# Optimization experiments

Measured on AMD Instinct MI355X. Metric: run time of the kernel, lower is better.

Reference implementation:

```python
import jax, jax.numpy as jnp
import numpy as np

WIN = (8, 8)
HEADS = 6
DIM = 192
N_TOK = WIN[0] * WIN[1]


def _cpb_coords_table():
    # (2*Wh-1, 2*Ww-1, 2) log-spaced continuous relative coords, flattened to (T, 2)
    h = np.arange(-(WIN[0] - 1), WIN[0], dtype=np.float32)
    w = np.arange(-(WIN[1] - 1), WIN[1], dtype=np.float32)
    t = np.stack(np.meshgrid(h, w, indexing='ij'), axis=-1)
    t[..., 0] /= WIN[0] - 1
    t[..., 1] /= WIN[1] - 1
    t *= 8.0
    t = np.sign(t) * np.log2(np.abs(t) + 1.0) / np.log2(8.0)
    return jnp.asarray(t.reshape(-1, 2))


def _rel_pos_index():
    ch, cw = np.meshgrid(np.arange(WIN[0]), np.arange(WIN[1]), indexing='ij')
    cf = np.stack([ch.ravel(), cw.ravel()])  # (2, N)
    rc = (cf[:, :, None] - cf[:, None, :]).transpose(1, 2, 0)  # (N, N, 2)
    rc[..., 0] += WIN[0] - 1
    rc[..., 1] += WIN[1] - 1
    rc[..., 0] *= 2 * WIN[1] - 1
    return jnp.asarray(rc.sum(-1).ravel())  # (N*N,)


_COORDS = _cpb_coords_table()
_RPI = _rel_pos_index()


def setup_inputs() -> dict:
    key = jax.random.key(0)
    ks = jax.random.split(key, 8)
    B_ = 4096
    x = jax.random.normal(ks[0], (B_, N_TOK, DIM), dtype=jnp.float32)
    mask = jnp.zeros((64, N_TOK, N_TOK), dtype=jnp.float32)
    qkv_w = jax.random.normal(ks[1], (3 * DIM, DIM), dtype=jnp.float32) * 0.02
    q_bias = jnp.zeros((DIM,), dtype=jnp.float32)
    v_bias = jnp.zeros((DIM,), dtype=jnp.float32)
    logit_scale = jnp.log(10.0) * jnp.ones((HEADS, 1, 1), dtype=jnp.float32)
    cpb_w1 = jax.random.normal(ks[2], (512, 2), dtype=jnp.float32) * 0.02
    cpb_b1 = jnp.zeros((512,), dtype=jnp.float32)
    cpb_w2 = jax.random.normal(ks[3], (HEADS, 512), dtype=jnp.float32) * 0.02
    proj_w = jax.random.normal(ks[4], (DIM, DIM), dtype=jnp.float32) * 0.02
    proj_b = jnp.zeros((DIM,), dtype=jnp.float32)
    return {"x": x, "mask": mask, "qkv_w": qkv_w, "q_bias": q_bias, "v_bias": v_bias,
            "logit_scale": logit_scale, "cpb_w1": cpb_w1, "cpb_b1": cpb_b1,
            "cpb_w2": cpb_w2, "proj_w": proj_w, "proj_b": proj_b}


def reference(x, mask, qkv_w, q_bias, v_bias, logit_scale, cpb_w1, cpb_b1, cpb_w2, proj_w, proj_b):
    B, N, C = x.shape
    H = HEADS
    d = C // H
    # qkv projection; bias layout matches torch.stack((q_bias, 0, v_bias)).view(3*C)
    qkv_bias = jnp.concatenate([q_bias, jnp.zeros_like(v_bias), v_bias])
    qkv = (x @ qkv_w.T + qkv_bias).reshape(B, N, 3, H, d).transpose(2, 0, 3, 1, 4)
    q, k, v = qkv[0], qkv[1], qkv[2]  # (B, H, N, d)
    # cosine attention: L2-normalize q, k (F.normalize with eps=1e-12)
    qn = q / jnp.maximum(jnp.linalg.norm(q, axis=-1, keepdims=True), 1e-12)
    kn = k / jnp.maximum(jnp.linalg.norm(k, axis=-1, keepdims=True), 1e-12)
    attn = jnp.einsum('bhnd,bhmd->bhnm', qn, kn)
    scale = jnp.exp(jnp.minimum(logit_scale, jnp.log(100.0)))  # clamp at 1/0.01
    attn = attn * scale  # (H,1,1) broadcasts over (B,H,N,N)
    # continuous position bias: MLP(2->512->H) on log-coords, gathered per pair
    tbl = jax.nn.relu(_COORDS @ cpb_w1.T + cpb_b1) @ cpb_w2.T  # (T, H)
    rpb = tbl[_RPI].reshape(N, N, H).transpose(2, 0, 1)  # (H, N, N)
    attn = attn + 16.0 * jax.nn.sigmoid(rpb)[None]
    nW = mask.shape[0]
    attn = attn.reshape(B // nW, nW, H, N, N) + mask[None, :, None]
    attn = jax.nn.softmax(attn.reshape(B, H, N, N), axis=-1)
    out = jnp.einsum('bhnm,bhmd->bhnd', attn, v).transpose(0, 2, 1, 3).reshape(B, N, C)
    return out @ proj_w.T + proj_b
```

## Files before the change

### kernel.cpp

```cpp
#include <hip/hip_runtime.h>
#include <math.h>

typedef __bf16 bf16_t;
typedef __bf16 bf16x8_t __attribute__((ext_vector_type(8)));
typedef __bf16 bf16x4_t __attribute__((ext_vector_type(4)));
typedef float f32x4_t __attribute__((ext_vector_type(4)));

#define MFMA(a, b, c) __builtin_amdgcn_mfma_f32_16x16x32_bf16((a), (b), (c), 0, 0, 0)

#define WS_WQKV 0u
#define WS_WPROJ 221184u
#define WS_QBIAS 294912u
#define WS_SCALE 297216u
#define WS_TBL 297472u
#define WS_BIAS16 303104u

__global__ __launch_bounds__(64) void cpb_table_kernel(
    const float* __restrict__ w1, const float* __restrict__ b1,
    const float* __restrict__ w2, float* __restrict__ tbl) {
  int t = blockIdx.x;
  int lane = threadIdx.x;
  int dh = t / 15 - 7, dw = t % 15 - 7;
  float th = (float)dh * (8.0f / 7.0f);
  float tw = (float)dw * (8.0f / 7.0f);
  float c0 = copysignf(log2f(fabsf(th) + 1.0f) / 3.0f, th);
  float c1 = copysignf(log2f(fabsf(tw) + 1.0f) / 3.0f, tw);
  float acc[6] = {0.f, 0.f, 0.f, 0.f, 0.f, 0.f};
  for (int k = lane; k < 512; k += 64) {
    float hv = fmaxf(w1[2 * k] * c0 + w1[2 * k + 1] * c1 + b1[k], 0.0f);
#pragma unroll
    for (int hh = 0; hh < 6; ++hh) acc[hh] += hv * w2[hh * 512 + k];
  }
#pragma unroll
  for (int hh = 0; hh < 6; ++hh) {
#pragma unroll
    for (int m = 1; m < 64; m <<= 1) acc[hh] += __shfl_xor(acc[hh], m, 64);
  }
  if (lane == 0) {
#pragma unroll
    for (int hh = 0; hh < 6; ++hh) tbl[t * 6 + hh] = acc[hh];
  }
}

__global__ __launch_bounds__(256) void prep_kernel(
    const float* __restrict__ qkv_w, const float* __restrict__ proj_w,
    const float* __restrict__ q_bias, const float* __restrict__ v_bias,
    const float* __restrict__ logit_scale, const float* __restrict__ tbl,
    bf16_t* __restrict__ wqkv, bf16_t* __restrict__ wproj,
    float* __restrict__ qbias, float* __restrict__ scalev,
    float* __restrict__ bias16) {
  int id = blockIdx.x * 256 + threadIdx.x;
  if (id < 110592) {
    wqkv[id] = (bf16_t)qkv_w[id];
  } else if (id < 147456) {
    int i = id - 110592;
    wproj[i] = (bf16_t)proj_w[i];
  } else if (id < 148032) {
    int i = id - 147456;
    float bv = (i < 192) ? q_bias[i] : ((i < 384) ? 0.0f : v_bias[i - 384]);
    qbias[i] = bv;
  } else if (id < 148038) {
    int hh = id - 148032;
    scalev[hh] = expf(fminf(logit_scale[hh], logf(100.0f)));
  } else if (id < 172614) {
    int i = id - 148038;
    int hh = i >> 12;
    int nm = i & 4095;
    int n = nm >> 6, m = nm & 63;
    int i1 = n >> 3, j1 = n & 7, i2 = m >> 3, j2 = m & 7;
    int rpi = (i1 - i2 + 7) * 15 + (j1 - j2 + 7);
    float v = tbl[rpi * 6 + hh];
    bias16[i] = 16.0f / (1.0f + __expf(-v));
  }
}

__global__ __launch_bounds__(768) void wattn_kernel(
    const float* __restrict__ x, const float* __restrict__ mask,
    const bf16_t* __restrict__ wqkv, const bf16_t* __restrict__ wproj,
    const float* __restrict__ qbias, const float* __restrict__ scalev,
    const float* __restrict__ bias16, const float* __restrict__ proj_b,
    float* __restrict__ out, int nw) {
  __shared__ __align__(16) char smem[131072];
  bf16_t* xs = (bf16_t*)smem;
  bf16_t* qs = (bf16_t*)(smem + 25600);
  bf16_t* Ps = (bf16_t*)smem;
  bf16_t* ksv = (bf16_t*)(smem + 56320);
  bf16_t* os = (bf16_t*)(smem + 56320);
  bf16_t* vts = (bf16_t*)(smem + 87040);
  float* msk = (float*)(smem + 114688);

  const int tid = threadIdx.x;
  const int wave = tid >> 6, lane = tid & 63;
  const int h = wave >> 1, s = wave & 1;
  const int quad = lane >> 4, col = lane & 15;
  const int b = blockIdx.x;

  const float4* xg = (const float4*)(x + (size_t)b * 12288);
  for (int i = tid; i < 3072; i += 768) {
    float4 v = xg[i];
    int row = i / 48;
    int c = (i - row * 48) * 4;
    bf16x4_t pk = {(bf16_t)v.x, (bf16_t)v.y, (bf16_t)v.z, (bf16_t)v.w};
    *(bf16x4_t*)(xs + row * 200 + c) = pk;
  }
  const float* mg = mask + (size_t)(b % nw) * 4096;
  for (int i = tid; i < 4096; i += 768) msk[i] = mg[i];
  __syncthreads();

  const float sc_h = scalev[h];
  const int mrow0 = 32 * s + col;
  const int mrow1 = mrow0 + 16;
  const int koff = quad * 8;
  const f32x4_t zz = {0.f, 0.f, 0.f, 0.f};

  for (int g = 0; g < 3; ++g) {
    int nbase = g * 192 + h * 32;
    f32x4_t a00 = zz, a01 = zz, a10 = zz, a11 = zz;
#pragma unroll
    for (int kk = 0; kk < 6; ++kk) {
      int k0 = kk * 32 + koff;
      bf16x8_t fa0 = *(const bf16x8_t*)(xs + mrow0 * 200 + k0);
      bf16x8_t fa1 = *(const bf16x8_t*)(xs + mrow1 * 200 + k0);
      bf16x8_t fb0 = *(const bf16x8_t*)(wqkv + (size_t)(nbase + col) * 192 + k0);
      bf16x8_t fb1 = *(const bf16x8_t*)(wqkv + (size_t)(nbase + 16 + col) * 192 + k0);
      a00 = MFMA(fa0, fb0, a00);
      a01 = MFMA(fa0, fb1, a01);
      a10 = MFMA(fa1, fb0, a10);
      a11 = MFMA(fa1, fb1, a11);
    }
    float bn0 = qbias[nbase + col];
    float bn1 = qbias[nbase + 16 + col];
    if (g < 2) {
      float mult = (g == 0) ? sc_h : 1.0f;
      bf16_t* dst = ((g == 0) ? qs : ksv) + h * 2560;
#pragma unroll
      for (int mi2 = 0; mi2 < 2; ++mi2) {
        f32x4_t va = mi2 ? a10 : a00;
        f32x4_t vb = mi2 ? a11 : a01;
#pragma unroll
        for (int r = 0; r < 4; ++r) {
          float v0 = va[r] + bn0, v1 = vb[r] + bn1;
          float ss = v0 * v0 + v1 * v1;
          ss += __shfl_xor(ss, 1, 64);
          ss += __shfl_xor(ss, 2, 64);
          ss += __shfl_xor(ss, 4, 64);
          ss += __shfl_xor(ss, 8, 64);
          float inv = mult / fmaxf(sqrtf(ss), 1e-12f);
          int token = (2 * s + mi2) * 16 + quad * 4 + r;
          dst[token * 40 + col] = (bf16_t)(v0 * inv);
          dst[token * 40 + 16 + col] = (bf16_t)(v1 * inv);
        }
      }
    } else {
      bf16_t* dst = vts + h * 2304;
#pragma unroll
      for (int mi2 = 0; mi2 < 2; ++mi2) {
        f32x4_t va = mi2 ? a10 : a00;
        f32x4_t vb = mi2 ? a11 : a01;
#pragma unroll
        for (int r = 0; r < 4; ++r) {
          int token = (2 * s + mi2) * 16 + quad * 4 + r;
          dst[col * 72 + token] = (bf16_t)(va[r] + bn0);
          dst[(16 + col) * 72 + token] = (bf16_t)(vb[r] + bn1);
        }
      }
    }
  }
  __syncthreads();

  f32x4_t at[2][4];
  {
    const bf16_t* qh = qs + h * 2560;
    const bf16_t* kh = ksv + h * 2560;
    bf16x8_t aq0 = *(const bf16x8_t*)(qh + mrow0 * 40 + koff);
    bf16x8_t aq1 = *(const bf16x8_t*)(qh + mrow1 * 40 + koff);
#pragma unroll
    for (int ni = 0; ni < 4; ++ni) {
      bf16x8_t bk = *(const bf16x8_t*)(kh + (ni * 16 + col) * 40 + koff);
      at[0][ni] = MFMA(aq0, bk, zz);
      at[1][ni] = MFMA(aq1, bk, zz);
    }
  }

  float p[2][4][4];
  const float* bg = bias16 + h * 4096;
#pragma unroll
  for (int mi2 = 0; mi2 < 2; ++mi2) {
#pragma unroll
    for (int r = 0; r < 4; ++r) {
      int m = (2 * s + mi2) * 16 + quad * 4 + r;
      float vals[4];
#pragma unroll
      for (int ni = 0; ni < 4; ++ni) {
        int n = ni * 16 + col;
        vals[ni] = at[mi2][ni][r] + bg[m * 64 + n] + msk[m * 64 + n];
      }
      float mx = fmaxf(fmaxf(vals[0], vals[1]), fmaxf(vals[2], vals[3]));
      mx = fmaxf(mx, __shfl_xor(mx, 1, 64));
      mx = fmaxf(mx, __shfl_xor(mx, 2, 64));
      mx = fmaxf(mx, __shfl_xor(mx, 4, 64));
      mx = fmaxf(mx, __shfl_xor(mx, 8, 64));
      float sm = 0.f;
#pragma unroll
      for (int ni = 0; ni < 4; ++ni) {
        vals[ni] = __expf(vals[ni] - mx);
        sm += vals[ni];
      }
      sm += __shfl_xor(sm, 1, 64);
      sm += __shfl_xor(sm, 2, 64);
      sm += __shfl_xor(sm, 4, 64);
      sm += __shfl_xor(sm, 8, 64);
      float inv = 1.0f / sm;
#pragma unroll
      for (int ni = 0; ni < 4; ++ni) p[mi2][ni][r] = vals[ni] * inv;
    }
  }
  __syncthreads();

  bf16_t* Ph = Ps + h * 4608;
#pragma unroll
  for (int mi2 = 0; mi2 < 2; ++mi2) {
#pragma unroll
    for (int ni = 0; ni < 4; ++ni) {
#pragma unroll
      for (int r = 0; r < 4; ++r) {
        int m = (2 * s + mi2) * 16 + quad * 4 + r;
        Ph[m * 72 + ni * 16 + col] = (bf16_t)p[mi2][ni][r];
      }
    }
  }

  f32x4_t oac[2][2] = {{zz, zz}, {zz, zz}};
  {
    const bf16_t* vh = vts + h * 2304;
#pragma unroll
    for (int kk = 0; kk < 2; ++kk) {
      int k0 = kk * 32 + koff;
      bf16x8_t pa0 = *(const bf16x8_t*)(Ph + mrow0 * 72 + k0);
      bf16x8_t pa1 = *(const bf16x8_t*)(Ph + mrow1 * 72 + k0);
      bf16x8_t vb0 = *(const bf16x8_t*)(vh + col * 72 + k0);
      bf16x8_t vb1 = *(const bf16x8_t*)(vh + (16 + col) * 72 + k0);
      oac[0][0] = MFMA(pa0, vb0, oac[0][0]);
      oac[0][1] = MFMA(pa0, vb1, oac[0][1]);
      oac[1][0] = MFMA(pa1, vb0, oac[1][0]);
      oac[1][1] = MFMA(pa1, vb1, oac[1][1]);
    }
  }
#pragma unroll
  for (int mi2 = 0; mi2 < 2; ++mi2) {
#pragma unroll
    for (int ni = 0; ni < 2; ++ni) {
#pragma unroll
      for (int r = 0; r < 4; ++r) {
        int token = (2 * s + mi2) * 16 + quad * 4 + r;
        os[token * 200 + h * 32 + ni * 16 + col] = (bf16_t)oac[mi2][ni][r];
      }
    }
  }
  __syncthreads();

  f32x4_t pr[2][2] = {{zz, zz}, {zz, zz}};
#pragma unroll
  for (int kk = 0; kk < 6; ++kk) {
    int k0 = kk * 32 + koff;
    bf16x8_t fa0 = *(const bf16x8_t*)(os + mrow0 * 200 + k0);
    bf16x8_t fa1 = *(const bf16x8_t*)(os + mrow1 * 200 + k0);
    bf16x8_t fb0 = *(const bf16x8_t*)(wproj + (size_t)(h * 32 + col) * 192 + k0);
    bf16x8_t fb1 = *(const bf16x8_t*)(wproj + (size_t)(h * 32 + 16 + col) * 192 + k0);
    pr[0][0] = MFMA(fa0, fb0, pr[0][0]);
    pr[0][1] = MFMA(fa0, fb1, pr[0][1]);
    pr[1][0] = MFMA(fa1, fb0, pr[1][0]);
    pr[1][1] = MFMA(fa1, fb1, pr[1][1]);
  }
  float pb0 = proj_b[h * 32 + col];
  float pb1 = proj_b[h * 32 + 16 + col];
  float* og = out + (size_t)b * 12288;
#pragma unroll
  for (int mi2 = 0; mi2 < 2; ++mi2) {
#pragma unroll
    for (int r = 0; r < 4; ++r) {
      int token = (2 * s + mi2) * 16 + quad * 4 + r;
      og[token * 192 + h * 32 + col] = pr[mi2][0][r] + pb0;
      og[token * 192 + h * 32 + 16 + col] = pr[mi2][1][r] + pb1;
    }
  }
}

extern "C" void kernel_launch(void* const* d_in, const int* in_sizes, int n_in,
                              void* d_out, int out_size, void* d_ws, size_t ws_size,
                              hipStream_t stream) {
  const float* x = (const float*)d_in[0];
  const float* mask = (const float*)d_in[1];
  const float* qkv_w = (const float*)d_in[2];
  const float* q_bias = (const float*)d_in[3];
  const float* v_bias = (const float*)d_in[4];
  const float* logit_scale = (const float*)d_in[5];
  const float* cpb_w1 = (const float*)d_in[6];
  const float* cpb_b1 = (const float*)d_in[7];
  const float* cpb_w2 = (const float*)d_in[8];
  const float* proj_w = (const float*)d_in[9];
  const float* proj_b = (const float*)d_in[10];
  float* out = (float*)d_out;

  char* ws = (char*)d_ws;
  bf16_t* wqkv = (bf16_t*)(ws + WS_WQKV);
  bf16_t* wproj = (bf16_t*)(ws + WS_WPROJ);
  float* qbias = (float*)(ws + WS_QBIAS);
  float* scalev = (float*)(ws + WS_SCALE);
  float* tbl = (float*)(ws + WS_TBL);
  float* bias16 = (float*)(ws + WS_BIAS16);

  const int nwin = in_sizes[0] / 12288;
  const int nw = in_sizes[1] / 4096;

  cpb_table_kernel<<<dim3(225), dim3(64), 0, stream>>>(cpb_w1, cpb_b1, cpb_w2, tbl);
  prep_kernel<<<dim3(675), dim3(256), 0, stream>>>(qkv_w, proj_w, q_bias, v_bias,
                                                   logit_scale, tbl, wqkv, wproj,
                                                   qbias, scalev, bias16);
  wattn_kernel<<<dim3(nwin), dim3(768), 0, stream>>>(x, mask, wqkv, wproj, qbias,
                                                     scalev, bias16, proj_b, out, nw);
}
```

Measured before the change: 703.7 us.

## Halve block size, process heads in two rounds, keep softmax probabilities in registers

The attention kernel now runs 384 threads. Each wave pair handles three heads in two rounds, which cuts LDS from 128KB to about 74KB so that more blocks can share a CU. Scores are computed transposed (K·Q) so each lane softmaxes along keys with only cross-quad shuffles. P is repacked into the MFMA operand layout through lane shuffles instead of an LDS round trip. The mask is stored in LDS as transposed bf16, the bias table is pre-transposed, and the output projection is retiled per wave. The costs are more register pressure from holding outputs across rounds, an extra barrier, bf16 rounding of the mask, and a prep launch that fills far more bias entries than the kernel uses.

```diff
diff --git a/kernel.cpp b/kernel.cpp
--- a/kernel.cpp
+++ b/kernel.cpp
@@ -5,6 +5,7 @@
 typedef __bf16 bf16x8_t __attribute__((ext_vector_type(8)));
 typedef __bf16 bf16x4_t __attribute__((ext_vector_type(4)));
 typedef float f32x4_t __attribute__((ext_vector_type(4)));
+typedef int i32x4_t __attribute__((ext_vector_type(4)));
 
 #define MFMA(a, b, c) __builtin_amdgcn_mfma_f32_16x16x32_bf16((a), (b), (c), 0, 0, 0)
 
@@ -13,7 +14,13 @@
 #define WS_QBIAS 294912u
 #define WS_SCALE 297216u
 #define WS_TBL 297472u
-#define WS_BIAS16 303104u
+#define WS_B16T 303104u
+
+static __device__ __forceinline__ unsigned pk2(float a, float b) {
+  unsigned short ua = __builtin_bit_cast(unsigned short, (bf16_t)a);
+  unsigned short ub = __builtin_bit_cast(unsigned short, (bf16_t)b);
+  return (unsigned)ua | ((unsigned)ub << 16);
+}
 
 __global__ __launch_bounds__(64) void cpb_table_kernel(
     const float* __restrict__ w1, const float* __restrict__ b1,
@@ -48,7 +55,7 @@
     const float* __restrict__ logit_scale, const float* __restrict__ tbl,
     bf16_t* __restrict__ wqkv, bf16_t* __restrict__ wproj,
     float* __restrict__ qbias, float* __restrict__ scalev,
-    float* __restrict__ bias16) {
+    float* __restrict__ b16T) {
   int id = blockIdx.x * 256 + threadIdx.x;
   if (id < 110592) {
     wqkv[id] = (bf16_t)qkv_w[id];
@@ -62,228 +69,255 @@
   } else if (id < 148038) {
     int hh = id - 148032;
     scalev[hh] = expf(fminf(logit_scale[hh], logf(100.0f)));
-  } else if (id < 172614) {
+  } else if (id < 246342) {
     int i = id - 148038;
     int hh = i >> 12;
-    int nm = i & 4095;
-    int n = nm >> 6, m = nm & 63;
-    int i1 = n >> 3, j1 = n & 7, i2 = m >> 3, j2 = m & 7;
+    int key = (i >> 6) & 63;
+    int n = i & 63;
+    int i1 = n >> 3, j1 = n & 7, i2 = key >> 3, j2 = key & 7;
     int rpi = (i1 - i2 + 7) * 15 + (j1 - j2 + 7);
     float v = tbl[rpi * 6 + hh];
-    bias16[i] = 16.0f / (1.0f + __expf(-v));
-  }
-}
-
-__global__ __launch_bounds__(768) void wattn_kernel(
+    b16T[i] = 16.0f / (1.0f + __expf(-v));
+  }
+}
+
+__global__ __launch_bounds__(384, 3) void wattn_kernel(
     const float* __restrict__ x, const float* __restrict__ mask,
     const bf16_t* __restrict__ wqkv, const bf16_t* __restrict__ wproj,
     const float* __restrict__ qbias, const float* __restrict__ scalev,
-    const float* __restrict__ bias16, const float* __restrict__ proj_b,
+    const float* __restrict__ b16T, const float* __restrict__ proj_b,
     float* __restrict__ out, int nw) {
-  __shared__ __align__(16) char smem[131072];
+  __shared__ __align__(16) char smem[75776];
   bf16_t* xs = (bf16_t*)smem;
-  bf16_t* qs = (bf16_t*)(smem + 25600);
-  bf16_t* Ps = (bf16_t*)smem;
-  bf16_t* ksv = (bf16_t*)(smem + 56320);
-  bf16_t* os = (bf16_t*)(smem + 56320);
-  bf16_t* vts = (bf16_t*)(smem + 87040);
-  float* msk = (float*)(smem + 114688);
+  bf16_t* qk = (bf16_t*)(smem + 25600);
+  bf16_t* vts = (bf16_t*)(smem + 53248);
+  bf16_t* mskT = (bf16_t*)(smem + 67072);
+  bf16_t* os = (bf16_t*)smem;
 
   const int tid = threadIdx.x;
   const int wave = tid >> 6, lane = tid & 63;
-  const int h = wave >> 1, s = wave & 1;
+  const int h3 = wave >> 1, s = wave & 1;
   const int quad = lane >> 4, col = lane & 15;
   const int b = blockIdx.x;
+  const bool hi32 = (lane & 32) != 0;
+  const int psrc0 = ((lane & 16) << 1) + col;
+  const int psrc1 = psrc0 + 16;
+  const f32x4_t zz = {0.f, 0.f, 0.f, 0.f};
 
   const float4* xg = (const float4*)(x + (size_t)b * 12288);
-  for (int i = tid; i < 3072; i += 768) {
+#pragma unroll
+  for (int it = 0; it < 8; ++it) {
+    int i = it * 384 + tid;
     float4 v = xg[i];
     int row = i / 48;
     int c = (i - row * 48) * 4;
-    bf16x4_t pk = {(bf16_t)v.x, (bf16_t)v.y, (bf16_t)v.z, (bf16_t)v.w};
-    *(bf16x4_t*)(xs + row * 200 + c) = pk;
+    bf16x4_t pkv = {(bf16_t)v.x, (bf16_t)v.y, (bf16_t)v.z, (bf16_t)v.w};
+    *(bf16x4_t*)(xs + row * 200 + c) = pkv;
   }
   const float* mg = mask + (size_t)(b % nw) * 4096;
-  for (int i = tid; i < 4096; i += 768) msk[i] = mg[i];
+  for (int i = tid; i < 4096; i += 384) {
+    int n = i >> 6, m = i & 63;
+    mskT[m * 68 + n] = (bf16_t)mg[i];
+  }
   __syncthreads();
 
-  const float sc_h = scalev[h];
-  const int mrow0 = 32 * s + col;
-  const int mrow1 = mrow0 + 16;
-  const int koff = quad * 8;
-  const f32x4_t zz = {0.f, 0.f, 0.f, 0.f};
-
-  for (int g = 0; g < 3; ++g) {
-    int nbase = g * 192 + h * 32;
-    f32x4_t a00 = zz, a01 = zz, a10 = zz, a11 = zz;
-#pragma unroll
-    for (int kk = 0; kk < 6; ++kk) {
-      int k0 = kk * 32 + koff;
-      bf16x8_t fa0 = *(const bf16x8_t*)(xs + mrow0 * 200 + k0);
-      bf16x8_t fa1 = *(const bf16x8_t*)(xs + mrow1 * 200 + k0);
-      bf16x8_t fb0 = *(const bf16x8_t*)(wqkv + (size_t)(nbase + col) * 192 + k0);
-      bf16x8_t fb1 = *(const bf16x8_t*)(wqkv + (size_t)(nbase + 16 + col) * 192 + k0);
-      a00 = MFMA(fa0, fb0, a00);
-      a01 = MFMA(fa0, fb1, a01);
-      a10 = MFMA(fa1, fb0, a10);
-      a11 = MFMA(fa1, fb1, a11);
-    }
-    float bn0 = qbias[nbase + col];
-    float bn1 = qbias[nbase + 16 + col];
-    if (g < 2) {
-      float mult = (g == 0) ? sc_h : 1.0f;
-      bf16_t* dst = ((g == 0) ? qs : ksv) + h * 2560;
-#pragma unroll
-      for (int mi2 = 0; mi2 < 2; ++mi2) {
-        f32x4_t va = mi2 ? a10 : a00;
-        f32x4_t vb = mi2 ? a11 : a01;
-#pragma unroll
-        for (int r = 0; r < 4; ++r) {
-          float v0 = va[r] + bn0, v1 = vb[r] + bn1;
-          float ss = v0 * v0 + v1 * v1;
-          ss += __shfl_xor(ss, 1, 64);
-          ss += __shfl_xor(ss, 2, 64);
-          ss += __shfl_xor(ss, 4, 64);
-          ss += __shfl_xor(ss, 8, 64);
-          float inv = mult / fmaxf(sqrtf(ss), 1e-12f);
-          int token = (2 * s + mi2) * 16 + quad * 4 + r;
-          dst[token * 40 + col] = (bf16_t)(v0 * inv);
-          dst[token * 40 + 16 + col] = (bf16_t)(v1 * inv);
+  f32x4_t oheld[2][2][2];
+  bf16_t* qkh = qk + h3 * 4608;
+  bf16_t* vtsh = vts + h3 * 2304;
+
+#pragma unroll
+  for (int r = 0; r < 2; ++r) {
+    const int h = r * 3 + h3;
+    if (r == 1) __syncthreads();
+    const float sc_h = scalev[h];
+
+#pragma unroll
+    for (int g = 0; g < 3; ++g) {
+      const int nbase = g * 192 + h * 32;
+      f32x4_t a00 = zz, a01 = zz, a10 = zz, a11 = zz;
+      const bf16_t* wb = wqkv + (size_t)nbase * 192;
+#pragma unroll
+      for (int kk = 0; kk < 6; ++kk) {
+        const int k0 = kk * 32 + quad * 8;
+        bf16x8_t fa0 = *(const bf16x8_t*)(xs + (s * 32 + col) * 200 + k0);
+        bf16x8_t fa1 = *(const bf16x8_t*)(xs + (s * 32 + 16 + col) * 200 + k0);
+        bf16x8_t fb0 = *(const bf16x8_t*)(wb + (size_t)col * 192 + k0);
+        bf16x8_t fb1 = *(const bf16x8_t*)(wb + (size_t)(16 + col) * 192 + k0);
+        a00 = MFMA(fa0, fb0, a00);
+        a01 = MFMA(fa0, fb1, a01);
+        a10 = MFMA(fa1, fb0, a10);
+        a11 = MFMA(fa1, fb1, a11);
+      }
+      float bn0 = qbias[nbase + col];
+      float bn1 = qbias[nbase + 16 + col];
+      if (g < 2) {
+        float mult = (g == 0) ? sc_h : 1.0f;
+        const int goff = g * 32;
+#pragma unroll
+        for (int mt = 0; mt < 2; ++mt) {
+          f32x4_t va = mt ? a10 : a00;
+          f32x4_t vb = mt ? a11 : a01;
+#pragma unroll
+          for (int rr = 0; rr < 4; ++rr) {
+            float v0 = va[rr] + bn0, v1 = vb[rr] + bn1;
+            float ss2 = v0 * v0 + v1 * v1;
+            ss2 += __shfl_xor(ss2, 1, 64);
+            ss2 += __shfl_xor(ss2, 2, 64);
+            ss2 += __shfl_xor(ss2, 4, 64);
+            ss2 += __shfl_xor(ss2, 8, 64);
+            float inv = mult / fmaxf(sqrtf(ss2), 1e-12f);
+            int token = s * 32 + mt * 16 + quad * 4 + rr;
+            qkh[token * 72 + goff + col] = (bf16_t)(v0 * inv);
+            qkh[token * 72 + goff + 16 + col] = (bf16_t)(v1 * inv);
+          }
         }
-      }
-    } else {
-      bf16_t* dst = vts + h * 2304;
-#pragma unroll
-      for (int mi2 = 0; mi2 < 2; ++mi2) {
-        f32x4_t va = mi2 ? a10 : a00;
-        f32x4_t vb = mi2 ? a11 : a01;
-#pragma unroll
-        for (int r = 0; r < 4; ++r) {
-          int token = (2 * s + mi2) * 16 + quad * 4 + r;
-          dst[col * 72 + token] = (bf16_t)(va[r] + bn0);
-          dst[(16 + col) * 72 + token] = (bf16_t)(vb[r] + bn1);
+      } else {
+#pragma unroll
+        for (int mt = 0; mt < 2; ++mt) {
+          f32x4_t va = mt ? a10 : a00;
+          f32x4_t vb = mt ? a11 : a01;
+          int tb = s * 32 + mt * 16 + quad * 4;
+          bf16x4_t p0 = {(bf16_t)(va[0] + bn0), (bf16_t)(va[1] + bn0),
+                         (bf16_t)(va[2] + bn0), (bf16_t)(va[3] + bn0)};
+          bf16x4_t p1 = {(bf16_t)(vb[0] + bn1), (bf16_t)(vb[1] + bn1),
+                         (bf16_t)(vb[2] + bn1), (bf16_t)(vb[3] + bn1)};
+          *(bf16x4_t*)(vtsh + col * 72 + tb) = p0;
+          *(bf16x4_t*)(vtsh + (16 + col) * 72 + tb) = p1;
         }
       }
     }
+    __syncthreads();
+
+    f32x4_t sacc[4][2];
+    {
+      bf16x8_t qf0 = *(const bf16x8_t*)(qkh + (s * 32 + col) * 72 + quad * 8);
+      bf16x8_t qf1 = *(const bf16x8_t*)(qkh + (s * 32 + 16 + col) * 72 + quad * 8);
+#pragma unroll
+      for (int mt = 0; mt < 4; ++mt) {
+        bf16x8_t kf = *(const bf16x8_t*)(qkh + (mt * 16 + col) * 72 + 32 + quad * 8);
+        sacc[mt][0] = MFMA(kf, qf0, zz);
+        sacc[mt][1] = MFMA(kf, qf1, zz);
+      }
+    }
+
+    const float* bT = b16T + h * 4096;
+    float pv[4][2][4];
+#pragma unroll
+    for (int nt = 0; nt < 2; ++nt) {
+      int qg = s * 32 + nt * 16 + col;
+      float vals[16];
+#pragma unroll
+      for (int mt = 0; mt < 4; ++mt)
+#pragma unroll
+        for (int rr = 0; rr < 4; ++rr) {
+          int key = mt * 16 + quad * 4 + rr;
+          vals[mt * 4 + rr] = sacc[mt][nt][rr] + bT[key * 64 + qg] + (float)mskT[key * 68 + qg];
+        }
+      float mx = vals[0];
+#pragma unroll
+      for (int i = 1; i < 16; ++i) mx = fmaxf(mx, vals[i]);
+      mx = fmaxf(mx, __shfl_xor(mx, 16, 64));
+      mx = fmaxf(mx, __shfl_xor(mx, 32, 64));
+      float sm = 0.f;
+#pragma unroll
+      for (int i = 0; i < 16; ++i) {
+        vals[i] = __expf(vals[i] - mx);
+        sm += vals[i];
+      }
+      sm += __shfl_xor(sm, 16, 64);
+      sm += __shfl_xor(sm, 32, 64);
+      float inv = 1.0f / sm;
+#pragma unroll
+      for (int mt = 0; mt < 4; ++mt)
+#pragma unroll
+        for (int rr = 0; rr < 4; ++rr) pv[mt][nt][rr] = vals[mt * 4 + rr] * inv;
+    }
+
+    unsigned pk01[4][2], pk23[4][2];
+#pragma unroll
+    for (int mt = 0; mt < 4; ++mt)
+#pragma unroll
+      for (int nt = 0; nt < 2; ++nt) {
+        pk01[mt][nt] = pk2(pv[mt][nt][0], pv[mt][nt][1]);
+        pk23[mt][nt] = pk2(pv[mt][nt][2], pv[mt][nt][3]);
+      }
+
+    f32x4_t oc[2][2] = {{zz, zz}, {zz, zz}};
+#pragma unroll
+    for (int kk = 0; kk < 2; ++kk) {
+      bf16x8_t bq[2];
+#pragma unroll
+      for (int nt = 0; nt < 2; ++nt) {
+        unsigned a0 = __shfl(pk01[kk * 2][nt], psrc0, 64);
+        unsigned b0 = __shfl(pk01[kk * 2 + 1][nt], psrc0, 64);
+        unsigned a1 = __shfl(pk23[kk * 2][nt], psrc0, 64);
+        unsigned b1 = __shfl(pk23[kk * 2 + 1][nt], psrc0, 64);
+        unsigned a2 = __shfl(pk01[kk * 2][nt], psrc1, 64);
+        unsigned b2 = __shfl(pk01[kk * 2 + 1][nt], psrc1, 64);
+        unsigned a3 = __shfl(pk23[kk * 2][nt], psrc1, 64);
+        unsigned b3 = __shfl(pk23[kk * 2 + 1][nt], psrc1, 64);
+        i32x4_t di = {(int)(hi32 ? b0 : a0), (int)(hi32 ? b1 : a1),
+                      (int)(hi32 ? b2 : a2), (int)(hi32 ? b3 : a3)};
+        bq[nt] = __builtin_bit_cast(bf16x8_t, di);
+      }
+#pragma unroll
+      for (int ct = 0; ct < 2; ++ct) {
+        bf16x8_t vf = *(const bf16x8_t*)(vtsh + (ct * 16 + col) * 72 + kk * 32 + quad * 8);
+        oc[ct][0] = MFMA(vf, bq[0], oc[ct][0]);
+        oc[ct][1] = MFMA(vf, bq[1], oc[ct][1]);
+      }
+    }
+#pragma unroll
+    for (int ct = 0; ct < 2; ++ct)
+#pragma unroll
+      for (int nt = 0; nt < 2; ++nt) oheld[r][ct][nt] = oc[ct][nt];
+  }
+
+#pragma unroll
+  for (int r2 = 0; r2 < 2; ++r2) {
+    int hh = r2 * 3 + h3;
+#pragma unroll
+    for (int ct = 0; ct < 2; ++ct)
+#pragma unroll
+      for (int nt = 0; nt < 2; ++nt) {
+        f32x4_t o = oheld[r2][ct][nt];
+        int token = s * 32 + nt * 16 + col;
+        int cb = hh * 32 + ct * 16 + quad * 4;
+        bf16x4_t pkk = {(bf16_t)o[0], (bf16_t)o[1], (bf16_t)o[2], (bf16_t)o[3]};
+        *(bf16x4_t*)(os + token * 200 + cb) = pkk;
+      }
   }
   __syncthreads();
 
-  f32x4_t at[2][4];
-  {
-    const bf16_t* qh = qs + h * 2560;
-    const bf16_t* kh = ksv + h * 2560;
-    bf16x8_t aq0 = *(const bf16x8_t*)(qh + mrow0 * 40 + koff);
-    bf16x8_t aq1 = *(const bf16x8_t*)(qh + mrow1 * 40 + koff);
-#pragma unroll
-    for (int ni = 0; ni < 4; ++ni) {
-      bf16x8_t bk = *(const bf16x8_t*)(kh + (ni * 16 + col) * 40 + koff);
-      at[0][ni] = MFMA(aq0, bk, zz);
-      at[1][ni] = MFMA(aq1, bk, zz);
-    }
-  }
-
-  float p[2][4][4];
-  const float* bg = bias16 + h * 4096;
-#pragma unroll
-  for (int mi2 = 0; mi2 < 2; ++mi2) {
-#pragma unroll
-    for (int r = 0; r < 4; ++r) {
-      int m = (2 * s + mi2) * 16 + quad * 4 + r;
-      float vals[4];
-#pragma unroll
-      for (int ni = 0; ni < 4; ++ni) {
-        int n = ni * 16 + col;
-        vals[ni] = at[mi2][ni][r] + bg[m * 64 + n] + msk[m * 64 + n];
-      }
-      float mx = fmaxf(fmaxf(vals[0], vals[1]), fmaxf(vals[2], vals[3]));
-      mx = fmaxf(mx, __shfl_xor(mx, 1, 64));
-      mx = fmaxf(mx, __shfl_xor(mx, 2, 64));
-      mx = fmaxf(mx, __shfl_xor(mx, 4, 64));
-      mx = fmaxf(mx, __shfl_xor(mx, 8, 64));
-      float sm = 0.f;
-#pragma unroll
-      for (int ni = 0; ni < 4; ++ni) {
-        vals[ni] = __expf(vals[ni] - mx);
-        sm += vals[ni];
-      }
-      sm += __shfl_xor(sm, 1, 64);
-      sm += __shfl_xor(sm, 2, 64);
-      sm += __shfl_xor(sm, 4, 64);
-      sm += __shfl_xor(sm, 8, 64);
-      float inv = 1.0f / sm;
-#pragma unroll
-      for (int ni = 0; ni < 4; ++ni) p[mi2][ni][r] = vals[ni] * inv;
-    }
-  }
-  __syncthreads();
-
-  bf16_t* Ph = Ps + h * 4608;
-#pragma unroll
-  for (int mi2 = 0; mi2 < 2; ++mi2) {
-#pragma unroll
-    for (int ni = 0; ni < 4; ++ni) {
-#pragma unroll
-      for (int r = 0; r < 4; ++r) {
-        int m = (2 * s + mi2) * 16 + quad * 4 + r;
-        Ph[m * 72 + ni * 16 + col] = (bf16_t)p[mi2][ni][r];
-      }
-    }
-  }
-
-  f32x4_t oac[2][2] = {{zz, zz}, {zz, zz}};
-  {
-    const bf16_t* vh = vts + h * 2304;
-#pragma unroll
-    for (int kk = 0; kk < 2; ++kk) {
-      int k0 = kk * 32 + koff;
-      bf16x8_t pa0 = *(const bf16x8_t*)(Ph + mrow0 * 72 + k0);
-      bf16x8_t pa1 = *(const bf16x8_t*)(Ph + mrow1 * 72 + k0);
-      bf16x8_t vb0 = *(const bf16x8_t*)(vh + col * 72 + k0);
-      bf16x8_t vb1 = *(const bf16x8_t*)(vh + (16 + col) * 72 + k0);
-      oac[0][0] = MFMA(pa0, vb0, oac[0][0]);
-      oac[0][1] = MFMA(pa0, vb1, oac[0][1]);
-      oac[1][0] = MFMA(pa1, vb0, oac[1][0]);
-      oac[1][1] = MFMA(pa1, vb1, oac[1][1]);
-    }
-  }
-#pragma unroll
-  for (int mi2 = 0; mi2 < 2; ++mi2) {
-#pragma unroll
-    for (int ni = 0; ni < 2; ++ni) {
-#pragma unroll
-      for (int r = 0; r < 4; ++r) {
-        int token = (2 * s + mi2) * 16 + quad * 4 + r;
-        os[token * 200 + h * 32 + ni * 16 + col] = (bf16_t)oac[mi2][ni][r];
-      }
-    }
-  }
-  __syncthreads();
-
-  f32x4_t pr[2][2] = {{zz, zz}, {zz, zz}};
+  const int cb = wave * 32;
+  f32x4_t pr[4][2];
+#pragma unroll
+  for (int mt = 0; mt < 4; ++mt) {
+    pr[mt][0] = zz;
+    pr[mt][1] = zz;
+  }
 #pragma unroll
   for (int kk = 0; kk < 6; ++kk) {
-    int k0 = kk * 32 + koff;
-    bf16x8_t fa0 = *(const bf16x8_t*)(os + mrow0 * 200 + k0);
-    bf16x8_t fa1 = *(const bf16x8_t*)(os + mrow1 * 200 + k0);
-    bf16x8_t fb0 = *(const bf16x8_t*)(wproj + (size_t)(h * 32 + col) * 192 + k0);
-    bf16x8_t fb1 = *(const bf16x8_t*)(wproj + (size_t)(h * 32 + 16 + col) * 192 + k0);
-    pr[0][0] = MFMA(fa0, fb0, pr[0][0]);
-    pr[0][1] = MFMA(fa0, fb1, pr[0][1]);
-    pr[1][0] = MFMA(fa1, fb0, pr[1][0]);
-    pr[1][1] = MFMA(fa1, fb1, pr[1][1]);
-  }
-  float pb0 = proj_b[h * 32 + col];
-  float pb1 = proj_b[h * 32 + 16 + col];
+    int k0 = kk * 32 + quad * 8;
+    bf16x8_t fb0 = *(const bf16x8_t*)(wproj + (size_t)(cb + col) * 192 + k0);
+    bf16x8_t fb1 = *(const bf16x8_t*)(wproj + (size_t)(cb + 16 + col) * 192 + k0);
+#pragma unroll
+    for (int mt = 0; mt < 4; ++mt) {
+      bf16x8_t fa = *(const bf16x8_t*)(os + (mt * 16 + col) * 200 + k0);
+      pr[mt][0] = MFMA(fa, fb0, pr[mt][0]);
+      pr[mt][1] = MFMA(fa, fb1, pr[mt][1]);
+    }
+  }
+  float pb0 = proj_b[cb + col], pb1 = proj_b[cb + 16 + col];
   float* og = out + (size_t)b * 12288;
 #pragma unroll
-  for (int mi2 = 0; mi2 < 2; ++mi2) {
-#pragma unroll
-    for (int r = 0; r < 4; ++r) {
-      int token = (2 * s + mi2) * 16 + quad * 4 + r;
-      og[token * 192 + h * 32 + col] = pr[mi2][0][r] + pb0;
-      og[token * 192 + h * 32 + 16 + col] = pr[mi2][1][r] + pb1;
-    }
-  }
+  for (int mt = 0; mt < 4; ++mt)
+#pragma unroll
+    for (int rr = 0; rr < 4; ++rr) {
+      int token = mt * 16 + quad * 4 + rr;
+      og[token * 192 + cb + col] = pr[mt][0][rr] + pb0;
+      og[token * 192 + cb + 16 + col] = pr[mt][1][rr] + pb1;
+    }
 }
 
 extern "C" void kernel_launch(void* const* d_in, const int* in_sizes, int n_in,
@@ -308,15 +342,15 @@
   float* qbias = (float*)(ws + WS_QBIAS);
   float* scalev = (float*)(ws + WS_SCALE);
   float* tbl = (float*)(ws + WS_TBL);
-  float* bias16 = (float*)(ws + WS_BIAS16);
+  float* b16T = (float*)(ws + WS_B16T);
 
   const int nwin = in_sizes[0] / 12288;
   const int nw = in_sizes[1] / 4096;
 
   cpb_table_kernel<<<dim3(225), dim3(64), 0, stream>>>(cpb_w1, cpb_b1, cpb_w2, tbl);
-  prep_kernel<<<dim3(675), dim3(256), 0, stream>>>(qkv_w, proj_w, q_bias, v_bias,
+  prep_kernel<<<dim3(963), dim3(256), 0, stream>>>(qkv_w, proj_w, q_bias, v_bias,
                                                    logit_scale, tbl, wqkv, wproj,
-                                                   qbias, scalev, bias16);
-  wattn_kernel<<<dim3(nwin), dim3(768), 0, stream>>>(x, mask, wqkv, wproj, qbias,
-                                                     scalev, bias16, proj_b, out, nw);
-}
+                                                   qbias, scalev, b16T);
+  wattn_kernel<<<dim3(nwin), dim3(384), 0, stream>>>(x, mask, wqkv, wproj, qbias,
+                                                     scalev, b16T, proj_b, out, nw);
+}
```

After: 916.3 us. +30.2%, slower.
